# Optimization experiments

Measured on AMD Instinct MI355X. Metric: run time of the kernel, lower is better.

Reference implementation:

```python
import jax, jax.numpy as jnp
import numpy as np

DIM = 768
H = 12          # num query heads
KV = 6          # num kv heads
GS = H // KV    # group size = 2
HD = DIM // H   # head dim = 64


def setup_inputs() -> dict:
    key = jax.random.key(0)
    ks = jax.random.split(key, 6)
    B, P = 8, 1024
    s = DIM ** -0.5
    x = jax.random.normal(ks[0], (B, P, DIM), dtype=jnp.float32)
    Wq = jax.random.normal(ks[1], (DIM, DIM), dtype=jnp.float32) * s
    Wk = jax.random.normal(ks[2], (DIM, KV * HD), dtype=jnp.float32) * s
    Wv = jax.random.normal(ks[3], (DIM, KV * HD), dtype=jnp.float32) * s
    Wp = jax.random.normal(ks[4], (DIM, DIM), dtype=jnp.float32) * s
    bp = jnp.zeros((DIM,), dtype=jnp.float32)
    return {"x": x, "Wq": Wq, "Wk": Wk, "Wv": Wv, "Wp": Wp, "bp": bp}


def reference(x, Wq, Wk, Wv, Wp, bp):
    B, P, C = x.shape
    scale = HD ** -0.5
    # projections; consecutive heads i*GS..(i+1)*GS-1 form kv-group i (torch.split dim=1)
    q = (x @ Wq).reshape(B, P, KV, GS, HD).transpose(0, 2, 3, 1, 4) * scale  # [B,KV,GS,P,d]
    k = (x @ Wk).reshape(B, P, KV, HD).transpose(0, 2, 1, 3)                 # [B,KV,P,d]
    v = (x @ Wv).reshape(B, P, KV, HD).transpose(0, 2, 1, 3)                 # [B,KV,P,d]

    scores = jnp.einsum('bghqd,bgkd->bghqk', q, k)      # [B,KV,GS,P,P]
    w = jax.nn.softmax(scores, axis=-1)                  # attn_drop=0 (eval)
    att = jnp.einsum('bghqk,bgkd->bghqd', w, v)          # [B,KV,GS,P,d]

    # per-group row-matched gaussian-ish noise (torch get_gaussian), vectorized over KV groups
    y = P * HD
    flat = att.reshape(B, KV, GS, y)                     # rows = groups within kv-group
    M = jax.random.uniform(jax.random.key(42), (KV, GS, y), dtype=flat.dtype)
    di = jnp.arange(min(GS, y))
    M = M.at[:, di, di].set(0.0)                         # sparse: zero diagonal
    m_mean = M.mean(axis=-1, keepdims=True)
    m_std = jnp.std(M, axis=-1, ddof=1, keepdims=True)   # torch.std is unbiased
    m_std = jnp.where(m_std == 0, jnp.ones_like(m_std), m_std)
    Z = (M - m_mean) / m_std                             # [KV,GS,y], shared across batch
    r_mean = flat.mean(axis=-1, keepdims=True)           # [B,KV,GS,1]
    r_std = jnp.std(flat, axis=-1, ddof=1, keepdims=True)
    flat = flat - (Z[None] * r_std + r_mean)

    att = flat.reshape(B, KV, GS, P, HD).reshape(B, H, P, HD)
    out = att.transpose(0, 2, 1, 3).reshape(B, P, C) @ Wp + bp  # proj_drop=0
    return out
```

## Files before the change

### kernel.cpp

```cpp
#include <hip/hip_runtime.h>
#include <hip/hip_bf16.h>
#include <math.h>


#define NTHREADS 256

typedef __bf16 bf16x8 __attribute__((ext_vector_type(8)));
typedef float f32x4 __attribute__((ext_vector_type(4)));

#define MFMA16(a, b, c) __builtin_amdgcn_mfma_f32_16x16x32_bf16(a, b, c, 0, 0, 0)

#define QSCALE 0.18033688011112042f

__device__ __forceinline__ float fexp2(float x) {
#if __has_builtin(__builtin_amdgcn_exp2f)
    return __builtin_amdgcn_exp2f(x);
#else
    return __expf(x * 0.6931471805599453f);
#endif
}

__device__ __forceinline__ void gload16(const void* g, void* l) {
    __builtin_amdgcn_global_load_lds(
        (const __attribute__((address_space(1))) void*)g,
        (__attribute__((address_space(3))) void*)l, 16, 0, 0);
}

__device__ __forceinline__ unsigned rotl_u32(unsigned x, int r) {
    return (x << r) | (x >> (32 - r));
}
__device__ __forceinline__ void threefry_0_42(unsigned x0, unsigned x1,
                                              unsigned& o0, unsigned& o1) {
    const unsigned ks0 = 0u, ks1 = 42u, ks2 = 0u ^ 42u ^ 0x1BD11BDAu;
    x0 += ks0; x1 += ks1;
#define R4(a,b,c,d) \
    x0 += x1; x1 = rotl_u32(x1,a); x1 ^= x0; \
    x0 += x1; x1 = rotl_u32(x1,b); x1 ^= x0; \
    x0 += x1; x1 = rotl_u32(x1,c); x1 ^= x0; \
    x0 += x1; x1 = rotl_u32(x1,d); x1 ^= x0;
    R4(13,15,26,6)   x0 += ks1; x1 += ks2 + 1u;
    R4(17,29,16,24)  x0 += ks2; x1 += ks0 + 2u;
    R4(13,15,26,6)   x0 += ks0; x1 += ks1 + 3u;
    R4(17,29,16,24)  x0 += ks1; x1 += ks2 + 4u;
    R4(13,15,26,6)   x0 += ks2; x1 += ks0 + 5u;
#undef R4
    o0 = x0; o1 = x1;
}
__device__ __forceinline__ float tf_uniform(unsigned i) {
    unsigned o0, o1;
    threefry_0_42(0u, i, o0, o1);
    unsigned bits = o0 ^ o1;
    return __uint_as_float((bits >> 9) | 0x3f800000u) - 1.0f;
}

__device__ __forceinline__ float wave_sum64(float v) {
#pragma unroll
    for (int off = 32; off; off >>= 1) v += __shfl_xor(v, off, 64);
    return v;
}

__device__ __forceinline__ unsigned short bf16_rne(float x) {
    unsigned u = __float_as_uint(x);
    return (unsigned short)((u + 0x7fffu + ((u >> 16) & 1u)) >> 16);
}
__device__ __forceinline__ unsigned pack_bf16x2(float lo, float hi) {
    return (unsigned)bf16_rne(lo) | ((unsigned)bf16_rne(hi) << 16);
}
__device__ __forceinline__ float bfu(unsigned v) {
    return __uint_as_float(v << 16);
}

__global__ __launch_bounds__(NTHREADS) void prep_k(
    const float* __restrict__ x, const float* __restrict__ Wq,
    const float* __restrict__ Wk, const float* __restrict__ Wv,
    const float* __restrict__ Wp,
    unsigned short* __restrict__ xb, unsigned short* __restrict__ wqt,
    unsigned short* __restrict__ wkt, unsigned short* __restrict__ wvt,
    unsigned short* __restrict__ wpt,
    unsigned short* __restrict__ zb, float* __restrict__ zpart)
{
    __shared__ float rbuf[8];
    int blk = blockIdx.x;
    if (blk < 1536) {
#pragma unroll
        for (int j = 0; j < 4; ++j) {
            int i = blk * 1024 + j * 256 + threadIdx.x;
            float4 v = ((const float4*)x)[i];
            uint2 u;
            u.x = pack_bf16x2(v.x, v.y);
            u.y = pack_bf16x2(v.z, v.w);
            *(uint2*)(xb + (size_t)i * 4) = u;
        }
    } else if (blk < 1920) {
        int zc = blk - 1536;
        int row = zc >> 5, chunk = zc & 31;
        int g = row & 1;
        int j0 = chunk * 2048;
        float sum = 0.f, sumsq = 0.f;
        for (int t = threadIdx.x; t < 2048; t += NTHREADS) {
            int j = j0 + t;
            unsigned i = (unsigned)row * 65536u + (unsigned)j;
            float m = tf_uniform(i);
            if (j == g) m = 0.f;
            zb[i] = bf16_rne(m);
            sum += m; sumsq += m * m;
        }
        sum = wave_sum64(sum); sumsq = wave_sum64(sumsq);
        int lane = threadIdx.x & 63, wv = threadIdx.x >> 6;
        if (lane == 0) { rbuf[wv] = sum; rbuf[4 + wv] = sumsq; }
        __syncthreads();
        if (threadIdx.x == 0) {
            zpart[zc * 2]     = rbuf[0] + rbuf[1] + rbuf[2] + rbuf[3];
            zpart[zc * 2 + 1] = rbuf[4] + rbuf[5] + rbuf[6] + rbuf[7];
        }
    } else {
        int id = blk - 1920;
        const float* W; unsigned short* Wt; int N;
        if (id < 144)      { W = Wq; Wt = wqt; N = 768; }
        else if (id < 216) { W = Wk; Wt = wkt; N = 384; id -= 144; }
        else if (id < 288) { W = Wv; Wt = wvt; N = 384; id -= 216; }
        else               { W = Wp; Wt = wpt; N = 768; id -= 288; }
        int ntn = N >> 6;
        int kt = id / ntn, nt = id % ntn;
        int k0 = kt * 64, n0 = nt * 64;
        int t = threadIdx.x;
        int tn = t & 63, tk = t >> 6;
        float r[16];
#pragma unroll
        for (int j = 0; j < 16; ++j)
            r[j] = W[(size_t)(k0 + tk * 16 + j) * N + n0 + tn];
        uint4 u0, u1;
        u0.x = pack_bf16x2(r[0], r[1]);   u0.y = pack_bf16x2(r[2], r[3]);
        u0.z = pack_bf16x2(r[4], r[5]);   u0.w = pack_bf16x2(r[6], r[7]);
        u1.x = pack_bf16x2(r[8], r[9]);   u1.y = pack_bf16x2(r[10], r[11]);
        u1.z = pack_bf16x2(r[12], r[13]); u1.w = pack_bf16x2(r[14], r[15]);
        unsigned short* dst = Wt + (size_t)(n0 + tn) * 768 + k0 + tk * 16;
        *(uint4*)dst = u0;
        *(uint4*)(dst + 8) = u1;
    }
}

__device__ __forceinline__ void mfma_tile64(
    const unsigned short* __restrict__ A, const unsigned short* __restrict__ Bt,
    int row0, int col0,
    unsigned short* As, unsigned short* Bs, f32x4 acc[4][2])
{
    const int tid = threadIdx.x;
    const int w = tid >> 6, lane = tid & 63;
    const int c = lane & 15, g = lane >> 4;

#pragma unroll
    for (int mi = 0; mi < 4; ++mi)
#pragma unroll
        for (int ni = 0; ni < 2; ++ni) acc[mi][ni] = (f32x4){0.f, 0.f, 0.f, 0.f};

    const unsigned short* gsrc[6];
    unsigned short* ldst[6];
#pragma unroll
    for (int j = 0; j < 6; ++j) {
        int seg = w * 6 + j;
        bool isA = seg < 8;
        int s = isA ? seg : seg - 8;
        int chunk = s >> 1, kh = s & 1;
        const unsigned short* gb = isA
            ? (A  + (size_t)(row0 + chunk * 16 + c) * 768)
            : (Bt + (size_t)(col0 + chunk * 16 + c) * 768);
        gsrc[j] = gb + kh * 32 + g * 8;
        ldst[j] = (isA ? As : Bs) + chunk * 1024 + kh * 512 + lane * 8;
    }

    for (int k0 = 0; k0 < 768; k0 += 64) {
        __syncthreads();
#pragma unroll
        for (int j = 0; j < 6; ++j) gload16(gsrc[j] + k0, ldst[j]);
        __syncthreads();
#pragma unroll
        for (int ks = 0; ks < 2; ++ks) {
            bf16x8 aA[4], bB[2];
#pragma unroll
            for (int mi = 0; mi < 4; ++mi)
                aA[mi] = *(const bf16x8*)&As[mi * 1024 + ks * 512 + g * 128 + c * 8];
#pragma unroll
            for (int ni = 0; ni < 2; ++ni)
                bB[ni] = *(const bf16x8*)&Bs[(w * 2 + ni) * 1024 + ks * 512 + g * 128 + c * 8];
#pragma unroll
            for (int mi = 0; mi < 4; ++mi)
#pragma unroll
                for (int ni = 0; ni < 2; ++ni)
                    acc[mi][ni] = MFMA16(aA[mi], bB[ni], acc[mi][ni]);
        }
    }
}

__global__ __launch_bounds__(NTHREADS) void qkv_mfma_k(
    const unsigned short* __restrict__ xb, const unsigned short* __restrict__ wqt,
    const unsigned short* __restrict__ wkt, const unsigned short* __restrict__ wvt,
    unsigned short* __restrict__ qbh, unsigned short* __restrict__ kb2,
    unsigned short* __restrict__ vb2)
{
    __shared__ unsigned short As[4096];
    __shared__ unsigned short Bs[8192];
    int id = blockIdx.x;
    int xcd = id & 7, slot = id >> 3;
    f32x4 acc[4][2];

    const int tid = threadIdx.x;
    const int w = tid >> 6, lane = tid & 63;
    const int c = lane & 15, g = lane >> 4;

    if (slot < 144) {
        int y0i = xcd + ((slot & 7) << 3);
        int nb = slot >> 3;
        int y0 = y0i * 128;
        bool isq = nb < 12;
        int row0 = isq ? nb * 64 : (nb - 12) * 64;
        const unsigned short* Wt = isq ? wqt : wkt;
        mfma_tile64(Wt, xb, row0, y0, As, Bs, acc);
        float scale = isq ? QSCALE : 1.0f;
#pragma unroll
        for (int mi = 0; mi < 4; ++mi) {
            int ocol = row0 + mi * 16 + g * 4;
#pragma unroll
            for (int ni = 0; ni < 2; ++ni) {
                int pglob = y0 + w * 32 + ni * 16 + c;
                int b = pglob >> 10, pin = pglob & 1023;
                ushort4 u;
                u.x = bf16_rne(acc[mi][ni][0] * scale);
                u.y = bf16_rne(acc[mi][ni][1] * scale);
                u.z = bf16_rne(acc[mi][ni][2] * scale);
                u.w = bf16_rne(acc[mi][ni][3] * scale);
                if (isq) {
                    int h = ocol >> 6, d0 = ocol & 63;
                    *(ushort4*)&qbh[(((size_t)b * 12 + h) * 1024 + pin) * 64 + d0] = u;
                } else {
                    int kv = ocol >> 6, d0 = ocol & 63;
                    int kt = pin >> 7, key = pin & 127;
                    *(ushort4*)&kb2[((((size_t)(b * 6 + kv) * 8 + kt) * 8 + (d0 >> 3)) * 128
                                     + key) * 8 + (d0 & 7)] = u;
                }
            }
        }
    } else {
        int s = slot - 144;
        int ct = s >> 4;
        int pt = xcd + ((s & 15) << 3);
        int row0 = pt * 64, col0 = ct * 128;
        mfma_tile64(xb, wvt, row0, col0, As, Bs, acc);
#pragma unroll
        for (int mi = 0; mi < 4; ++mi) {
            int pglob = row0 + mi * 16 + g * 4;
            int b = pglob >> 10, pin = pglob & 1023;
            int kt = pin >> 7, pg = (pin & 127) >> 3, p8 = pin & 7;
#pragma unroll
            for (int ni = 0; ni < 2; ++ni) {
                int vcol = col0 + w * 32 + ni * 16 + c;
                int kv = vcol >> 6, d = vcol & 63;
                ushort4 u;
                u.x = bf16_rne(acc[mi][ni][0]);
                u.y = bf16_rne(acc[mi][ni][1]);
                u.z = bf16_rne(acc[mi][ni][2]);
                u.w = bf16_rne(acc[mi][ni][3]);
                *(ushort4*)&vb2[((((size_t)(b * 6 + kv) * 8 + kt) * 16 + pg) * 64 + d) * 8 + p8] = u;
            }
        }
    }
}

__global__ __launch_bounds__(NTHREADS) void proj_mfma_k(
    const unsigned short* __restrict__ attb, const unsigned short* __restrict__ wpt,
    const float* __restrict__ bp, float* __restrict__ out)
{
    __shared__ unsigned short As[4096];
    __shared__ unsigned short Bs[8192];
    int id = blockIdx.x;
    int xcd = id & 7, slot = id >> 3;
    int col0i = xcd + ((slot & 7) << 3);
    int row0i = slot >> 3;
    int row0 = row0i * 64, col0 = col0i * 128;
    f32x4 acc[4][2];
    mfma_tile64(wpt, attb, row0, col0, As, Bs, acc);

    const int tid = threadIdx.x;
    const int w = tid >> 6, lane = tid & 63;
    const int c = lane & 15, g = lane >> 4;
#pragma unroll
    for (int mi = 0; mi < 4; ++mi) {
        int ocol = row0 + mi * 16 + g * 4;
        float4 bias = *(const float4*)&bp[ocol];
#pragma unroll
        for (int ni = 0; ni < 2; ++ni) {
            int p = col0 + w * 32 + ni * 16 + c;
            float4 u;
            u.x = acc[mi][ni][0] + bias.x;
            u.y = acc[mi][ni][1] + bias.y;
            u.z = acc[mi][ni][2] + bias.z;
            u.w = acc[mi][ni][3] + bias.w;
            *(float4*)&out[(size_t)p * 768 + ocol] = u;
        }
    }
}

#define LDP 136
__global__ __launch_bounds__(NTHREADS) void attn_mfma_k(
    const unsigned short* __restrict__ qbh, const unsigned short* __restrict__ kb2,
    const unsigned short* __restrict__ vb2, unsigned short* __restrict__ attb,
    float* __restrict__ spart)
{
    __shared__ unsigned short P_lds[4 * 32 * LDP];
    __shared__ float l_s[4][32];
    __shared__ float sbuf[8];

    int id = blockIdx.x;
    int xcd = id & 7, slot = id >> 3;
    int grp = slot % 6, member = slot / 6;
    int g48 = xcd + 8 * grp;
    int b = g48 / 6, kv = g48 % 6;
    int h = kv * 2 + (member & 1);
    int qtile = member >> 1;
    const int qt0 = qtile * 128;

    const int tid = threadIdx.x;
    const int w = tid >> 6, lane = tid & 63;
    const int c = lane & 15, g = lane >> 4;

    const unsigned short* qh = qbh + (((size_t)b * 12 + h) * 1024 + qt0 + w * 32) * 64;
    const unsigned short* kbase = kb2 + ((size_t)(b * 6 + kv) * 8) * 8192;
    const unsigned short* vbase = vb2 + ((size_t)(b * 6 + kv) * 8) * 8192;
    unsigned short* Pw = P_lds + w * 32 * LDP;

    bf16x8 bQ[2][2];
#pragma unroll
    for (int ks = 0; ks < 2; ++ks) {
        bQ[ks][0] = *(const bf16x8*)(qh + (size_t)(c) * 64 + ks * 32 + g * 8);
        bQ[ks][1] = *(const bf16x8*)(qh + (size_t)(16 + c) * 64 + ks * 32 + g * 8);
    }

    f32x4 O[2][4];
#pragma unroll
    for (int i = 0; i < 2; ++i)
#pragma unroll
        for (int j = 0; j < 4; ++j) O[i][j] = (f32x4){0.f, 0.f, 0.f, 0.f};
    float l_r[2] = {0.f, 0.f};

    for (int t = 0; t < 8; ++t) {
        const unsigned short* kt = kbase + (size_t)t * 8192;
        const unsigned short* vt = vbase + (size_t)t * 8192;

        bf16x8 aK[2][8];
#pragma unroll
        for (int ks = 0; ks < 2; ++ks)
#pragma unroll
            for (int mb = 0; mb < 8; ++mb)
                aK[ks][mb] = *(const bf16x8*)(kt + ((size_t)(ks * 4 + g) * 128 + mb * 16 + c) * 8);

        f32x4 S[8][2];
#pragma unroll
        for (int mb = 0; mb < 8; ++mb) {
            S[mb][0] = (f32x4){0.f, 0.f, 0.f, 0.f};
            S[mb][1] = (f32x4){0.f, 0.f, 0.f, 0.f};
        }
#pragma unroll
        for (int ks = 0; ks < 2; ++ks)
#pragma unroll
            for (int mb = 0; mb < 8; ++mb) {
                S[mb][0] = MFMA16(aK[ks][mb], bQ[ks][0], S[mb][0]);
                S[mb][1] = MFMA16(aK[ks][mb], bQ[ks][1], S[mb][1]);
            }

        bf16x8 bV[4][4];
#pragma unroll
        for (int ks = 0; ks < 4; ++ks)
#pragma unroll
            for (int nb = 0; nb < 4; ++nb)
                bV[ks][nb] = *(const bf16x8*)(vt + ((size_t)(ks * 4 + g) * 64 + nb * 16 + c) * 8);

#pragma unroll
        for (int qn = 0; qn < 2; ++qn) {
            float lt = 0.f;
#pragma unroll
            for (int mb = 0; mb < 8; ++mb) {
                float p0 = fexp2(S[mb][qn][0]);
                float p1 = fexp2(S[mb][qn][1]);
                float p2 = fexp2(S[mb][qn][2]);
                float p3 = fexp2(S[mb][qn][3]);
                lt += (p0 + p1) + (p2 + p3);
                uint2 uu;
                uu.x = pack_bf16x2(p0, p1);
                uu.y = pack_bf16x2(p2, p3);
                *(uint2*)&Pw[(size_t)(qn * 16 + c) * LDP + mb * 16 + g * 4] = uu;
            }
            lt += __shfl_xor(lt, 16, 64);
            lt += __shfl_xor(lt, 32, 64);
            l_r[qn] += lt;
        }

#pragma unroll
        for (int ks = 0; ks < 4; ++ks) {
            bf16x8 aP0 = *(const bf16x8*)&Pw[(size_t)(c) * LDP + ks * 32 + g * 8];
            bf16x8 aP1 = *(const bf16x8*)&Pw[(size_t)(16 + c) * LDP + ks * 32 + g * 8];
#pragma unroll
            for (int nb = 0; nb < 4; ++nb) {
                O[0][nb] = MFMA16(aP0, bV[ks][nb], O[0][nb]);
                O[1][nb] = MFMA16(aP1, bV[ks][nb], O[1][nb]);
            }
        }
    }
    if (g == 0) { l_s[w][c] = l_r[0]; l_s[w][16 + c] = l_r[1]; }
    f32x4 li0 = *(f32x4*)&l_s[w][g * 4];
    f32x4 li1 = *(f32x4*)&l_s[w][16 + g * 4];
    float inv0[4], inv1[4];
#pragma unroll
    for (int r = 0; r < 4; ++r) { inv0[r] = 1.f / li0[r]; inv1[r] = 1.f / li1[r]; }
    unsigned short* ob = attb + ((size_t)b * 1024 + qt0 + w * 32) * 768 + h * 64;
    float psum = 0.f, psumsq = 0.f;
#pragma unroll
    for (int r = 0; r < 4; ++r) {
#pragma unroll
        for (int nb = 0; nb < 4; ++nb) {
            float o0 = O[0][nb][r] * inv0[r];
            float o1 = O[1][nb][r] * inv1[r];
            psum += o0 + o1;
            psumsq += o0 * o0 + o1 * o1;
            ob[(size_t)(g * 4 + r) * 768 + nb * 16 + c]      = bf16_rne(o0);
            ob[(size_t)(16 + g * 4 + r) * 768 + nb * 16 + c] = bf16_rne(o1);
        }
    }
    psum = wave_sum64(psum); psumsq = wave_sum64(psumsq);
    if (lane == 0) { sbuf[w] = psum; sbuf[4 + w] = psumsq; }
    __syncthreads();
    if (tid == 0) {
        int idx = ((b * 12 + h) * 8 + qtile) * 2;
        spart[idx]     = sbuf[0] + sbuf[1] + sbuf[2] + sbuf[3];
        spart[idx + 1] = sbuf[4] + sbuf[5] + sbuf[6] + sbuf[7];
    }
}

__global__ __launch_bounds__(NTHREADS) void stats2_k(
    unsigned short* __restrict__ attb, const unsigned short* __restrict__ zb,
    const float* __restrict__ spart, const float* __restrict__ zpart)
{
    int blk = blockIdx.x;
    int bh = blk >> 3, ch = blk & 7;
    int b = bh / 12, h = bh % 12;
    float zs = 0.f, zs2 = 0.f, rs = 0.f, rs2 = 0.f;
#pragma unroll
    for (int cc = 0; cc < 32; ++cc) {
        zs  += zpart[(h * 32 + cc) * 2];
        zs2 += zpart[(h * 32 + cc) * 2 + 1];
    }
#pragma unroll
    for (int cc = 0; cc < 8; ++cc) {
        rs  += spart[(bh * 8 + cc) * 2];
        rs2 += spart[(bh * 8 + cc) * 2 + 1];
    }
    float m_mean = zs * (1.f / 65536.f);
    float m_var  = (zs2 - 65536.f * m_mean * m_mean) * (1.f / 65535.f);
    float m_sd   = sqrtf(fmaxf(m_var, 0.f));
    if (m_sd == 0.f) m_sd = 1.f;
    float r_mean = rs * (1.f / 65536.f);
    float r_var  = (rs2 - 65536.f * r_mean * r_mean) * (1.f / 65535.f);
    float r_sd   = sqrtf(fmaxf(r_var, 0.f));
    float a = r_sd / m_sd;
    float bc = m_mean * a - r_mean;

    unsigned short* base = attb + ((size_t)b * 1024 + ch * 128) * 768 + h * 64;
    const unsigned short* zrow = zb + (size_t)h * 65536 + (size_t)ch * 8192;
    for (int f = threadIdx.x; f < 1024; f += NTHREADS) {
        int p = f >> 3, dq = (f & 7) * 8;
        unsigned short* ptr = base + (size_t)p * 768 + dq;
        uint4 u = *(const uint4*)ptr;
        uint4 zu = *(const uint4*)(zrow + (size_t)f * 8);
        float v0 = bfu(u.x)       - bfu(zu.x)       * a + bc;
        float v1 = bfu(u.x >> 16) - bfu(zu.x >> 16) * a + bc;
        float v2 = bfu(u.y)       - bfu(zu.y)       * a + bc;
        float v3 = bfu(u.y >> 16) - bfu(zu.y >> 16) * a + bc;
        float v4 = bfu(u.z)       - bfu(zu.z)       * a + bc;
        float v5 = bfu(u.z >> 16) - bfu(zu.z >> 16) * a + bc;
        float v6 = bfu(u.w)       - bfu(zu.w)       * a + bc;
        float v7 = bfu(u.w >> 16) - bfu(zu.w >> 16) * a + bc;
        uint4 o;
        o.x = pack_bf16x2(v0, v1);
        o.y = pack_bf16x2(v2, v3);
        o.z = pack_bf16x2(v4, v5);
        o.w = pack_bf16x2(v6, v7);
        *(uint4*)ptr = o;
    }
}

extern "C" void kernel_launch(void* const* d_in, const int* in_sizes, int n_in,
                              void* d_out, int out_size, void* d_ws, size_t ws_size,
                              hipStream_t stream) {
    const float* x  = (const float*)d_in[0];
    const float* Wq = (const float*)d_in[1];
    const float* Wk = (const float*)d_in[2];
    const float* Wv = (const float*)d_in[3];
    const float* Wp = (const float*)d_in[4];
    const float* bp = (const float*)d_in[5];
    float* out = (float*)d_out;

    float* ws    = (float*)d_ws;
    float* zpart = ws;
    float* spart = zpart + 768;
    unsigned short* zb   = (unsigned short*)(spart + 1536);
    unsigned short* xb   = zb + 786432;
    unsigned short* wqt  = xb + 6291456;
    unsigned short* wkt  = wqt + 589824;
    unsigned short* wvt  = wkt + 294912;
    unsigned short* wpt  = wvt + 294912;
    unsigned short* qbh  = wpt + 589824;
    unsigned short* kb2  = qbh + 6291456;
    unsigned short* vb2  = kb2 + 3145728;
    unsigned short* attb = vb2 + 3145728;

    prep_k<<<2352, NTHREADS, 0, stream>>>(x, Wq, Wk, Wv, Wp,
                                          xb, wqt, wkt, wvt, wpt, zb, zpart);
    qkv_mfma_k<<<1536, NTHREADS, 0, stream>>>(xb, wqt, wkt, wvt, qbh, kb2, vb2);
    attn_mfma_k<<<768, NTHREADS, 0, stream>>>(qbh, kb2, vb2, attb, spart);
    stats2_k<<<768, NTHREADS, 0, stream>>>(attb, zb, spart, zpart);
    proj_mfma_k<<<768, NTHREADS, 0, stream>>>(attb, wpt, bp, out);
}
```

Measured before the change: 230.0 us.

## Use 128x256 MFMA GEMM tiles and fuse Q/K/V into one stacked-weight GEMM

Replaces the 64x128 GEMM tile with a 128x256 tile run by 512 threads (8 waves in a 2x4 layout), raising the data reuse of each LDS load for both the QKV and output projection kernels. The QKV kernel now treats the contiguous wqt/wkt/wvt buffers as one stacked 1536x768 weight and picks the Q, K or V output layout per row block. This removes the separate V-branch orientation. The trade-offs are fewer blocks (384 and 192), which can leave CUs idle on the proj GEMM, and V results now written with scalar strided stores.

Result: no change. 230.4 us (+0.1%).

```diff
diff --git a/kernel.cpp b/kernel.cpp
--- a/kernel.cpp
+++ b/kernel.cpp
@@ -140,27 +140,28 @@
     }
 }
 
-__device__ __forceinline__ void mfma_tile64(
+__device__ __forceinline__ void mfma_tile128x256(
     const unsigned short* __restrict__ A, const unsigned short* __restrict__ Bt,
     int row0, int col0,
-    unsigned short* As, unsigned short* Bs, f32x4 acc[4][2])
+    unsigned short* As, unsigned short* Bs, f32x4 acc[4][4])
 {
     const int tid = threadIdx.x;
     const int w = tid >> 6, lane = tid & 63;
     const int c = lane & 15, g = lane >> 4;
+    const int wm = w & 1, wn = w >> 1;
 
 #pragma unroll
     for (int mi = 0; mi < 4; ++mi)
 #pragma unroll
-        for (int ni = 0; ni < 2; ++ni) acc[mi][ni] = (f32x4){0.f, 0.f, 0.f, 0.f};
+        for (int ni = 0; ni < 4; ++ni) acc[mi][ni] = (f32x4){0.f, 0.f, 0.f, 0.f};
 
     const unsigned short* gsrc[6];
     unsigned short* ldst[6];
 #pragma unroll
     for (int j = 0; j < 6; ++j) {
         int seg = w * 6 + j;
-        bool isA = seg < 8;
-        int s = isA ? seg : seg - 8;
+        bool isA = seg < 16;
+        int s = isA ? seg : seg - 16;
         int chunk = s >> 1, kh = s & 1;
         const unsigned short* gb = isA
             ? (A  + (size_t)(row0 + chunk * 16 + c) * 768)
@@ -176,120 +177,108 @@
         __syncthreads();
 #pragma unroll
         for (int ks = 0; ks < 2; ++ks) {
-            bf16x8 aA[4], bB[2];
+            bf16x8 aA[4], bB[4];
 #pragma unroll
             for (int mi = 0; mi < 4; ++mi)
-                aA[mi] = *(const bf16x8*)&As[mi * 1024 + ks * 512 + g * 128 + c * 8];
-#pragma unroll
-            for (int ni = 0; ni < 2; ++ni)
-                bB[ni] = *(const bf16x8*)&Bs[(w * 2 + ni) * 1024 + ks * 512 + g * 128 + c * 8];
+                aA[mi] = *(const bf16x8*)&As[(wm * 4 + mi) * 1024 + ks * 512 + g * 128 + c * 8];
+#pragma unroll
+            for (int ni = 0; ni < 4; ++ni)
+                bB[ni] = *(const bf16x8*)&Bs[(wn * 4 + ni) * 1024 + ks * 512 + g * 128 + c * 8];
 #pragma unroll
             for (int mi = 0; mi < 4; ++mi)
 #pragma unroll
-                for (int ni = 0; ni < 2; ++ni)
+                for (int ni = 0; ni < 4; ++ni)
                     acc[mi][ni] = MFMA16(aA[mi], bB[ni], acc[mi][ni]);
         }
     }
 }
 
-__global__ __launch_bounds__(NTHREADS) void qkv_mfma_k(
-    const unsigned short* __restrict__ xb, const unsigned short* __restrict__ wqt,
-    const unsigned short* __restrict__ wkt, const unsigned short* __restrict__ wvt,
+__global__ __launch_bounds__(512) void qkv_mfma_k(
+    const unsigned short* __restrict__ xb, const unsigned short* __restrict__ wstk,
     unsigned short* __restrict__ qbh, unsigned short* __restrict__ kb2,
     unsigned short* __restrict__ vb2)
 {
-    __shared__ unsigned short As[4096];
-    __shared__ unsigned short Bs[8192];
+    __shared__ unsigned short As[8192];
+    __shared__ unsigned short Bs[16384];
     int id = blockIdx.x;
     int xcd = id & 7, slot = id >> 3;
-    f32x4 acc[4][2];
+    int col0i = xcd + ((slot & 3) << 3);
+    int row0i = slot >> 2;
+    int row0 = row0i * 128, col0 = col0i * 256;
+    f32x4 acc[4][4];
+    mfma_tile128x256(wstk, xb, row0, col0, As, Bs, acc);
 
     const int tid = threadIdx.x;
     const int w = tid >> 6, lane = tid & 63;
     const int c = lane & 15, g = lane >> 4;
-
-    if (slot < 144) {
-        int y0i = xcd + ((slot & 7) << 3);
-        int nb = slot >> 3;
-        int y0 = y0i * 128;
-        bool isq = nb < 12;
-        int row0 = isq ? nb * 64 : (nb - 12) * 64;
-        const unsigned short* Wt = isq ? wqt : wkt;
-        mfma_tile64(Wt, xb, row0, y0, As, Bs, acc);
-        float scale = isq ? QSCALE : 1.0f;
-#pragma unroll
-        for (int mi = 0; mi < 4; ++mi) {
-            int ocol = row0 + mi * 16 + g * 4;
-#pragma unroll
-            for (int ni = 0; ni < 2; ++ni) {
-                int pglob = y0 + w * 32 + ni * 16 + c;
-                int b = pglob >> 10, pin = pglob & 1023;
+    const int wm = w & 1, wn = w >> 1;
+
+#pragma unroll
+    for (int mi = 0; mi < 4; ++mi) {
+        int ocb = row0 + wm * 64 + mi * 16;
+        int ocol = ocb + g * 4;
+#pragma unroll
+        for (int ni = 0; ni < 4; ++ni) {
+            int pglob = col0 + wn * 64 + ni * 16 + c;
+            int b = pglob >> 10, pin = pglob & 1023;
+            if (ocb < 768) {
                 ushort4 u;
-                u.x = bf16_rne(acc[mi][ni][0] * scale);
-                u.y = bf16_rne(acc[mi][ni][1] * scale);
-                u.z = bf16_rne(acc[mi][ni][2] * scale);
-                u.w = bf16_rne(acc[mi][ni][3] * scale);
-                if (isq) {
-                    int h = ocol >> 6, d0 = ocol & 63;
-                    *(ushort4*)&qbh[(((size_t)b * 12 + h) * 1024 + pin) * 64 + d0] = u;
-                } else {
-                    int kv = ocol >> 6, d0 = ocol & 63;
-                    int kt = pin >> 7, key = pin & 127;
-                    *(ushort4*)&kb2[((((size_t)(b * 6 + kv) * 8 + kt) * 8 + (d0 >> 3)) * 128
-                                     + key) * 8 + (d0 & 7)] = u;
-                }
-            }
-        }
-    } else {
-        int s = slot - 144;
-        int ct = s >> 4;
-        int pt = xcd + ((s & 15) << 3);
-        int row0 = pt * 64, col0 = ct * 128;
-        mfma_tile64(xb, wvt, row0, col0, As, Bs, acc);
-#pragma unroll
-        for (int mi = 0; mi < 4; ++mi) {
-            int pglob = row0 + mi * 16 + g * 4;
-            int b = pglob >> 10, pin = pglob & 1023;
-            int kt = pin >> 7, pg = (pin & 127) >> 3, p8 = pin & 7;
-#pragma unroll
-            for (int ni = 0; ni < 2; ++ni) {
-                int vcol = col0 + w * 32 + ni * 16 + c;
-                int kv = vcol >> 6, d = vcol & 63;
+                u.x = bf16_rne(acc[mi][ni][0] * QSCALE);
+                u.y = bf16_rne(acc[mi][ni][1] * QSCALE);
+                u.z = bf16_rne(acc[mi][ni][2] * QSCALE);
+                u.w = bf16_rne(acc[mi][ni][3] * QSCALE);
+                int h = ocol >> 6, d0 = ocol & 63;
+                *(ushort4*)&qbh[(((size_t)b * 12 + h) * 1024 + pin) * 64 + d0] = u;
+            } else if (ocb < 1152) {
+                int kcol = ocol - 768;
+                int kv = kcol >> 6, d0 = kcol & 63;
+                int kt = pin >> 7, key = pin & 127;
                 ushort4 u;
                 u.x = bf16_rne(acc[mi][ni][0]);
                 u.y = bf16_rne(acc[mi][ni][1]);
                 u.z = bf16_rne(acc[mi][ni][2]);
                 u.w = bf16_rne(acc[mi][ni][3]);
-                *(ushort4*)&vb2[((((size_t)(b * 6 + kv) * 8 + kt) * 16 + pg) * 64 + d) * 8 + p8] = u;
+                *(ushort4*)&kb2[((((size_t)(b * 6 + kv) * 8 + kt) * 8 + (d0 >> 3)) * 128
+                                 + key) * 8 + (d0 & 7)] = u;
+            } else {
+                int kt = pin >> 7, pg = (pin & 127) >> 3, p8 = pin & 7;
+#pragma unroll
+                for (int r = 0; r < 4; ++r) {
+                    int vcol = ocol + r - 1152;
+                    int kv = vcol >> 6, d = vcol & 63;
+                    vb2[((((size_t)(b * 6 + kv) * 8 + kt) * 16 + pg) * 64 + d) * 8 + p8]
+                        = bf16_rne(acc[mi][ni][r]);
+                }
             }
         }
     }
 }
 
-__global__ __launch_bounds__(NTHREADS) void proj_mfma_k(
+__global__ __launch_bounds__(512) void proj_mfma_k(
     const unsigned short* __restrict__ attb, const unsigned short* __restrict__ wpt,
     const float* __restrict__ bp, float* __restrict__ out)
 {
-    __shared__ unsigned short As[4096];
-    __shared__ unsigned short Bs[8192];
+    __shared__ unsigned short As[8192];
+    __shared__ unsigned short Bs[16384];
     int id = blockIdx.x;
     int xcd = id & 7, slot = id >> 3;
-    int col0i = xcd + ((slot & 7) << 3);
-    int row0i = slot >> 3;
-    int row0 = row0i * 64, col0 = col0i * 128;
-    f32x4 acc[4][2];
-    mfma_tile64(wpt, attb, row0, col0, As, Bs, acc);
+    int col0i = xcd + ((slot & 3) << 3);
+    int row0i = slot >> 2;
+    int row0 = row0i * 128, col0 = col0i * 256;
+    f32x4 acc[4][4];
+    mfma_tile128x256(wpt, attb, row0, col0, As, Bs, acc);
 
     const int tid = threadIdx.x;
     const int w = tid >> 6, lane = tid & 63;
     const int c = lane & 15, g = lane >> 4;
+    const int wm = w & 1, wn = w >> 1;
 #pragma unroll
     for (int mi = 0; mi < 4; ++mi) {
-        int ocol = row0 + mi * 16 + g * 4;
+        int ocol = row0 + wm * 64 + mi * 16 + g * 4;
         float4 bias = *(const float4*)&bp[ocol];
 #pragma unroll
-        for (int ni = 0; ni < 2; ++ni) {
-            int p = col0 + w * 32 + ni * 16 + c;
+        for (int ni = 0; ni < 4; ++ni) {
+            int p = col0 + wn * 64 + ni * 16 + c;
             float4 u;
             u.x = acc[mi][ni][0] + bias.x;
             u.y = acc[mi][ni][1] + bias.y;
@@ -514,8 +503,8 @@
 
     prep_k<<<2352, NTHREADS, 0, stream>>>(x, Wq, Wk, Wv, Wp,
                                           xb, wqt, wkt, wvt, wpt, zb, zpart);
-    qkv_mfma_k<<<1536, NTHREADS, 0, stream>>>(xb, wqt, wkt, wvt, qbh, kb2, vb2);
+    qkv_mfma_k<<<384, 512, 0, stream>>>(xb, wqt, qbh, kb2, vb2);
     attn_mfma_k<<<768, NTHREADS, 0, stream>>>(qbh, kb2, vb2, attb, spart);
     stats2_k<<<768, NTHREADS, 0, stream>>>(attb, zb, spart, zpart);
-    proj_mfma_k<<<768, NTHREADS, 0, stream>>>(attb, wpt, bp, out);
-}
+    proj_mfma_k<<<192, 512, 0, stream>>>(attb, wpt, bp, out);
+}
```
